# Kernel optimization log

Hardware: AMD Instinct MI355X
Metric: run time of the kernel (lower is better)

## Reference

```python
import jax, jax.numpy as jnp
import numpy as np

E = 512
H = 8
D = E // H  # 64
B = 2
S = 4096


def setup_inputs() -> dict:
    key = jax.random.key(0)
    ks = jax.random.split(key, 12)
    s = 1.0 / np.sqrt(E)
    return {
        "x": jax.random.normal(ks[0], (B, S, E), dtype=jnp.float32),
        "bias": jax.random.normal(ks[1], (H, 1, S, S), dtype=jnp.float32),
        "mask": jax.random.randint(ks[2], (1, 1, S, S), 0, 2, dtype=jnp.int32),
        "Wq": jax.random.normal(ks[3], (E, E), dtype=jnp.float32) * s,
        "bq": jnp.zeros((E,), dtype=jnp.float32),
        "Wk": jax.random.normal(ks[4], (E, E), dtype=jnp.float32) * s,
        "bk": jnp.zeros((E,), dtype=jnp.float32),
        "Wv": jax.random.normal(ks[5], (E, E), dtype=jnp.float32) * s,
        "bv": jnp.zeros((E,), dtype=jnp.float32),
        "Wo": jax.random.normal(ks[6], (E, E), dtype=jnp.float32) * s,
        "bo": jnp.zeros((E,), dtype=jnp.float32),
    }


def _split_heads(t):
    # [B,S,E] -> [H,B,S,D]  (matches x.view(B,-1,H,D).permute(2,0,1,3))
    b, s, _ = t.shape
    return t.reshape(b, s, H, D).transpose(2, 0, 1, 3)


def reference(x, bias, mask, Wq, bq, Wk, bk, Wv, bv, Wo, bo):
    # torch Linear: y = x @ W.T + b
    q = _split_heads(x @ Wq.T + bq)  # [H,B,S,D]
    k = _split_heads(x @ Wk.T + bk)
    v = _split_heads(x @ Wv.T + bv)

    scores = jnp.einsum("hbqd,hbkd->hbqk", q, k) + bias  # [H,B,S,S]
    scores = jnp.where(mask == 0, jnp.float32(-1e20), scores)
    # NOTE: original divides AFTER bias-add and masking
    probs = jax.nn.softmax(scores / jnp.sqrt(jnp.float32(D)), axis=-1)
    out = jnp.einsum("hbqk,hbkd->hbqd", probs, v)  # [H,B,S,D]
    out = out.transpose(1, 2, 0, 3).reshape(x.shape[0], -1, H * D)  # [B,S,E]
    return out @ Wo.T + bo
```

## Files before the change

kernel.cpp:

```cpp
#include <hip/hip_runtime.h>
#include <hip/hip_bf16.h>

typedef __bf16 bf16x8 __attribute__((ext_vector_type(8)));
typedef float f32x4 __attribute__((ext_vector_type(4)));

#define S_LEN 4096
#define EMB   512
#define NHEAD 8
#define HDIM  64
#define NBAT  2
#define NROW  (NBAT * S_LEN)

static __device__ __forceinline__ f32x4 mfma16x16(bf16x8 a, bf16x8 b, f32x4 c) {
    return __builtin_amdgcn_mfma_f32_16x16x32_bf16(a, b, c, 0, 0, 0);
}

__global__ __launch_bounds__(256) void convert_kernel(
    const float* __restrict__ x, const float* __restrict__ Wq,
    const float* __restrict__ Wk, const float* __restrict__ Wv,
    const float* __restrict__ Wo,
    __hip_bfloat16* __restrict__ xb, __hip_bfloat16* __restrict__ wqkv,
    __hip_bfloat16* __restrict__ wob)
{
    const int NX = NROW * EMB;
    const int NW = EMB * EMB;
    int i = blockIdx.x * 256 + threadIdx.x;
    if (i < NX) { xb[i] = __float2bfloat16(x[i]); return; }
    int j = i - NX;
    if (j < 3 * NW) {
        int p = j >> 18, r = j & (NW - 1);
        const float* src = (p == 0) ? Wq : (p == 1) ? Wk : Wv;
        wqkv[j] = __float2bfloat16(src[r]);
    } else if (j < 4 * NW) {
        int r = j - 3 * NW;
        wob[r] = __float2bfloat16(Wo[r]);
    }
}

__device__ __forceinline__ void gemm_core(
    const __hip_bfloat16* __restrict__ A, const __hip_bfloat16* __restrict__ Bw,
    int mbase, int nbase,
    __hip_bfloat16* As, __hip_bfloat16* Bs, f32x4 acc[2][4])
{
    const int tid = threadIdx.x;
    const int w = tid >> 6, lane = tid & 63, l = lane & 15, quad = lane >> 4;
    const f32x4 zero = {0.f, 0.f, 0.f, 0.f};
#pragma unroll
    for (int mb = 0; mb < 2; mb++)
#pragma unroll
        for (int nb = 0; nb < 4; nb++) acc[mb][nb] = zero;

    const int r0 = tid >> 2, kc = tid & 3;
    const __hip_bfloat16* pa0 = A + (size_t)(mbase + r0) * EMB + kc * 8;
    const __hip_bfloat16* pa1 = pa0 + (size_t)64 * EMB;
    const __hip_bfloat16* pb  = Bw + (size_t)(nbase + r0) * EMB + kc * 8;

    uint4 va0 = *(const uint4*)pa0;
    uint4 va1 = *(const uint4*)pa1;
    uint4 vb  = *(const uint4*)pb;

    for (int k0 = 0; k0 < EMB; k0 += 32) {
        __syncthreads();
        *(uint4*)(As + r0 * 40 + kc * 8)        = va0;
        *(uint4*)(As + (r0 + 64) * 40 + kc * 8) = va1;
        *(uint4*)(Bs + r0 * 40 + kc * 8)        = vb;
        __syncthreads();
        if (k0 + 32 < EMB) {
            va0 = *(const uint4*)(pa0 + k0 + 32);
            va1 = *(const uint4*)(pa1 + k0 + 32);
            vb  = *(const uint4*)(pb  + k0 + 32);
        }
        bf16x8 af[2], bfr[4];
#pragma unroll
        for (int mb = 0; mb < 2; mb++)
            af[mb] = *(const bf16x8*)(As + (w * 32 + mb * 16 + l) * 40 + quad * 8);
#pragma unroll
        for (int nb = 0; nb < 4; nb++)
            bfr[nb] = *(const bf16x8*)(Bs + (nb * 16 + l) * 40 + quad * 8);
        __builtin_amdgcn_s_setprio(1);
#pragma unroll
        for (int mb = 0; mb < 2; mb++)
#pragma unroll
            for (int nb = 0; nb < 4; nb++)
                acc[mb][nb] = mfma16x16(af[mb], bfr[nb], acc[mb][nb]);
        __builtin_amdgcn_s_setprio(0);
    }
}

__global__ __launch_bounds__(256, 4) void qkv_gemm(
    const __hip_bfloat16* __restrict__ xb, const __hip_bfloat16* __restrict__ wqkv,
    const float* __restrict__ bq, const float* __restrict__ bk, const float* __restrict__ bv,
    __hip_bfloat16* __restrict__ Qh, __hip_bfloat16* __restrict__ Kh,
    __hip_bfloat16* __restrict__ Vt)
{
    __shared__ __align__(16) __hip_bfloat16 As[128 * 40];
    __shared__ __align__(16) __hip_bfloat16 Bs[64 * 40];
    const int mbase = blockIdx.x * 128, nbase = blockIdx.y * 64;
    f32x4 acc[2][4];
    gemm_core(xb, wqkv, mbase, nbase, As, Bs, acc);

    const int tid = threadIdx.x;
    const int w = tid >> 6, lane = tid & 63, l = lane & 15, quad = lane >> 4;
    const int p = nbase >> 9;
    const float* bias = (p == 0) ? bq : (p == 1) ? bk : bv;
    __hip_bfloat16* dst = (p == 0) ? Qh : (p == 1) ? Kh : Vt;
#pragma unroll
    for (int mb = 0; mb < 2; mb++)
#pragma unroll
        for (int nb = 0; nb < 4; nb++)
#pragma unroll
            for (int r = 0; r < 4; r++) {
                int m = mbase + w * 32 + mb * 16 + quad * 4 + r;
                int n = nbase + nb * 16 + l;
                int o = n & 511;
                float v = acc[mb][nb][r] + bias[o];
                int b = m >> 12, s = m & 4095, hh = o >> 6, d = o & 63;
                size_t idx = (p == 2)
                    ? ((size_t)((hh * 2 + b) * 64 + d)) * 4096 + s
                    : ((size_t)((hh * 2 + b) * 4096 + s)) * 64 + d;
                dst[idx] = __float2bfloat16(v);
            }
}

__global__ __launch_bounds__(256, 2) void attn_kernel(
    const __hip_bfloat16* __restrict__ Qh, const __hip_bfloat16* __restrict__ Kh,
    const __hip_bfloat16* __restrict__ Vt,
    const float* __restrict__ bias, const int* __restrict__ mask,
    __hip_bfloat16* __restrict__ Om)
{
    const int h = blockIdx.x, qt = blockIdx.y;
    const int tid = threadIdx.x;
    const int w = tid >> 6, lane = tid & 63, l = lane & 15, quad = lane >> 4;
    const int q0 = qt * 64;
    const float CS = 0.18033688011112042f;

    __shared__ __align__(16) __hip_bfloat16 Ks[2][64 * 72];
    __shared__ __align__(16) __hip_bfloat16 Vs[2][64 * 72];
    __shared__ __align__(16) __hip_bfloat16 Ps[64 * 72];

    bf16x8 qf[2][2];
#pragma unroll
    for (int b = 0; b < 2; b++) {
        const __hip_bfloat16* qp =
            Qh + ((size_t)((h * 2 + b) * 4096 + q0 + w * 16 + l)) * 64;
        qf[b][0] = *(const bf16x8*)(qp + quad * 8);
        qf[b][1] = *(const bf16x8*)(qp + 32 + quad * 8);
    }

    f32x4 oacc[2][4];
    float mst[2][4], lst[2][4];
    const f32x4 zero = {0.f, 0.f, 0.f, 0.f};
#pragma unroll
    for (int b = 0; b < 2; b++) {
#pragma unroll
        for (int nb = 0; nb < 4; nb++) oacc[b][nb] = zero;
#pragma unroll
        for (int r = 0; r < 4; r++) { mst[b][r] = -__builtin_inff(); lst[b][r] = 0.f; }
    }

    const __hip_bfloat16* kvsrc[8];
    __hip_bfloat16* kvdst[8];
#pragma unroll
    for (int j = 0; j < 8; j++) {
        int c = j * 256 + tid;
        int t = c >> 9, b = t & 1, isV = t >> 1;
        int cc = c & 511, row = cc >> 3, ch = cc & 7;
        if (isV) {
            kvsrc[j] = Vt + ((size_t)((h * 2 + b) * 64 + row)) * 4096 + ch * 8;
            kvdst[j] = Vs[b] + row * 72 + ch * 8;
        } else {
            kvsrc[j] = Kh + ((size_t)((h * 2 + b) * 4096 + row)) * 64 + ch * 8;
            kvdst[j] = Ks[b] + row * 72 + ch * 8;
        }
    }
    const float* bptr[4];
    const int*   mptr[4];
#pragma unroll
    for (int r = 0; r < 4; r++) {
        int qq = q0 + w * 16 + quad * 4 + r;
        bptr[r] = bias + (size_t)h * S_LEN * S_LEN + (size_t)qq * S_LEN + l;
        mptr[r] = mask + (size_t)qq * S_LEN + l;
    }

    uint4 kvbuf[8];
    float bb[4][4];
    int   mm[4][4];
#pragma unroll
    for (int j = 0; j < 8; j++) {
        kvbuf[j] = *(const uint4*)kvsrc[j];
        kvsrc[j] += (j >> 2) ? 64 : 64 * 64;
    }
#pragma unroll
    for (int nb = 0; nb < 4; nb++)
#pragma unroll
        for (int r = 0; r < 4; r++) {
            bb[nb][r] = bptr[r][nb * 16];
            mm[nb][r] = mptr[r][nb * 16];
        }
#pragma unroll
    for (int r = 0; r < 4; r++) { bptr[r] += 64; mptr[r] += 64; }

    for (int kt = 0; kt < 64; kt++) {
        __syncthreads();
#pragma unroll
        for (int j = 0; j < 8; j++) *(uint4*)kvdst[j] = kvbuf[j];
        float bor[4][4];
#pragma unroll
        for (int nb = 0; nb < 4; nb++)
#pragma unroll
            for (int r = 0; r < 4; r++)
                bor[nb][r] = mm[nb][r] ? bb[nb][r] : -1e30f;
        __syncthreads();

        if (kt < 63) {
#pragma unroll
            for (int j = 0; j < 8; j++) {
                kvbuf[j] = *(const uint4*)kvsrc[j];
                kvsrc[j] += (j >> 2) ? 64 : 64 * 64;
            }
#pragma unroll
            for (int nb = 0; nb < 4; nb++)
#pragma unroll
                for (int r = 0; r < 4; r++) {
                    bb[nb][r] = bptr[r][nb * 16];
                    mm[nb][r] = mptr[r][nb * 16];
                }
#pragma unroll
            for (int r = 0; r < 4; r++) { bptr[r] += 64; mptr[r] += 64; }
        }

#pragma unroll
        for (int b = 0; b < 2; b++) {
            f32x4 sc[4] = {zero, zero, zero, zero};
            __builtin_amdgcn_s_setprio(1);
#pragma unroll
            for (int ks = 0; ks < 2; ks++)
#pragma unroll
                for (int nb = 0; nb < 4; nb++) {
                    bf16x8 kf = *(const bf16x8*)(Ks[b] + (nb * 16 + l) * 72 + ks * 32 + quad * 8);
                    sc[nb] = mfma16x16(qf[b][ks], kf, sc[nb]);
                }
            __builtin_amdgcn_s_setprio(0);
            float xv[4][4], rmax[4];
#pragma unroll
            for (int r = 0; r < 4; r++) rmax[r] = -__builtin_inff();
#pragma unroll
            for (int nb = 0; nb < 4; nb++)
#pragma unroll
                for (int r = 0; r < 4; r++) {
                    xv[nb][r] = (sc[nb][r] + bor[nb][r]) * CS;
                    rmax[r] = fmaxf(rmax[r], xv[nb][r]);
                }
#pragma unroll
            for (int r = 0; r < 4; r++) {
                rmax[r] = fmaxf(rmax[r], __shfl_xor(rmax[r], 1));
                rmax[r] = fmaxf(rmax[r], __shfl_xor(rmax[r], 2));
                rmax[r] = fmaxf(rmax[r], __shfl_xor(rmax[r], 4));
                rmax[r] = fmaxf(rmax[r], __shfl_xor(rmax[r], 8));
            }
            float alpha[4], rsum[4];
#pragma unroll
            for (int r = 0; r < 4; r++) {
                float mn = fmaxf(mst[b][r], rmax[r]);
                alpha[r] = __builtin_amdgcn_exp2f(mst[b][r] - mn);
                mst[b][r] = mn;
                rsum[r] = 0.f;
            }
#pragma unroll
            for (int nb = 0; nb < 4; nb++)
#pragma unroll
                for (int r = 0; r < 4; r++) {
                    float e = __builtin_amdgcn_exp2f(xv[nb][r] - mst[b][r]);
                    rsum[r] += e;
                    Ps[(w * 16 + quad * 4 + r) * 72 + nb * 16 + l] =
                        __float2bfloat16(e);
                }
#pragma unroll
            for (int r = 0; r < 4; r++) {
                rsum[r] += __shfl_xor(rsum[r], 1);
                rsum[r] += __shfl_xor(rsum[r], 2);
                rsum[r] += __shfl_xor(rsum[r], 4);
                rsum[r] += __shfl_xor(rsum[r], 8);
                lst[b][r] = lst[b][r] * alpha[r] + rsum[r];
            }
#pragma unroll
            for (int nb = 0; nb < 4; nb++)
#pragma unroll
                for (int r = 0; r < 4; r++) oacc[b][nb][r] *= alpha[r];
            __builtin_amdgcn_s_setprio(1);
#pragma unroll
            for (int ks = 0; ks < 2; ks++) {
                bf16x8 pf = *(const bf16x8*)(Ps + (w * 16 + l) * 72 + ks * 32 + quad * 8);
#pragma unroll
                for (int nb = 0; nb < 4; nb++) {
                    bf16x8 vf = *(const bf16x8*)(Vs[b] + (nb * 16 + l) * 72 + ks * 32 + quad * 8);
                    oacc[b][nb] = mfma16x16(pf, vf, oacc[b][nb]);
                }
            }
            __builtin_amdgcn_s_setprio(0);
        }
    }

#pragma unroll
    for (int b = 0; b < 2; b++)
#pragma unroll
        for (int nb = 0; nb < 4; nb++)
#pragma unroll
            for (int r = 0; r < 4; r++) {
                int qq = q0 + w * 16 + quad * 4 + r;
                float val = oacc[b][nb][r] / lst[b][r];
                Om[((size_t)(b * 4096 + qq)) * 512 + h * 64 + nb * 16 + l] =
                    __float2bfloat16(val);
            }
}

__global__ __launch_bounds__(256, 4) void out_gemm(
    const __hip_bfloat16* __restrict__ Om, const __hip_bfloat16* __restrict__ wob,
    const float* __restrict__ bo, float* __restrict__ out)
{
    __shared__ __align__(16) __hip_bfloat16 As[128 * 40];
    __shared__ __align__(16) __hip_bfloat16 Bs[64 * 40];
    const int mbase = blockIdx.x * 128, nbase = blockIdx.y * 64;
    f32x4 acc[2][4];
    gemm_core(Om, wob, mbase, nbase, As, Bs, acc);

    const int tid = threadIdx.x;
    const int w = tid >> 6, lane = tid & 63, l = lane & 15, quad = lane >> 4;
#pragma unroll
    for (int mb = 0; mb < 2; mb++)
#pragma unroll
        for (int nb = 0; nb < 4; nb++)
#pragma unroll
            for (int r = 0; r < 4; r++) {
                int m = mbase + w * 32 + mb * 16 + quad * 4 + r;
                int n = nbase + nb * 16 + l;
                out[(size_t)m * EMB + n] = acc[mb][nb][r] + bo[n];
            }
}

extern "C" void kernel_launch(void* const* d_in, const int* in_sizes, int n_in,
                              void* d_out, int out_size, void* d_ws, size_t ws_size,
                              hipStream_t stream) {
    const float* x    = (const float*)d_in[0];
    const float* bias = (const float*)d_in[1];
    const int*   mask = (const int*)d_in[2];
    const float* Wq   = (const float*)d_in[3];
    const float* bq   = (const float*)d_in[4];
    const float* Wk   = (const float*)d_in[5];
    const float* bk   = (const float*)d_in[6];
    const float* Wv   = (const float*)d_in[7];
    const float* bv   = (const float*)d_in[8];
    const float* Wo   = (const float*)d_in[9];
    const float* bo   = (const float*)d_in[10];
    float* out = (float*)d_out;

    char* ws = (char*)d_ws;
    __hip_bfloat16* xb   = (__hip_bfloat16*)ws; ws += (size_t)NROW * EMB * 2;
    __hip_bfloat16* wqkv = (__hip_bfloat16*)ws; ws += (size_t)3 * EMB * EMB * 2;
    __hip_bfloat16* wob  = (__hip_bfloat16*)ws; ws += (size_t)EMB * EMB * 2;
    __hip_bfloat16* Qh   = (__hip_bfloat16*)ws; ws += (size_t)NROW * EMB * 2;
    __hip_bfloat16* Kh   = (__hip_bfloat16*)ws; ws += (size_t)NROW * EMB * 2;
    __hip_bfloat16* Vt   = (__hip_bfloat16*)ws; ws += (size_t)NROW * EMB * 2;
    __hip_bfloat16* Om   = (__hip_bfloat16*)ws; ws += (size_t)NROW * EMB * 2;

    convert_kernel<<<dim3(20480), dim3(256), 0, stream>>>(
        x, Wq, Wk, Wv, Wo, xb, wqkv, wob);
    qkv_gemm<<<dim3(64, 24), dim3(256), 0, stream>>>(
        xb, wqkv, bq, bk, bv, Qh, Kh, Vt);
    attn_kernel<<<dim3(NHEAD, 64), dim3(256), 0, stream>>>(
        Qh, Kh, Vt, bias, mask, Om);
    out_gemm<<<dim3(64, 8), dim3(256), 0, stream>>>(Om, wob, bo, out);
}
```

Measured before the change: 1.261 ms.

## Stage bias and mask through LDS with vectorized float4 loads

```diff
diff --git a/kernel.cpp b/kernel.cpp
--- a/kernel.cpp
+++ b/kernel.cpp
@@ -137,6 +137,7 @@
     __shared__ __align__(16) __hip_bfloat16 Ks[2][64 * 72];
     __shared__ __align__(16) __hip_bfloat16 Vs[2][64 * 72];
     __shared__ __align__(16) __hip_bfloat16 Ps[64 * 72];
+    __shared__ __align__(16) float Bor[64 * 68];
 
     bf16x8 qf[2][2];
 #pragma unroll
@@ -158,76 +159,78 @@
         for (int r = 0; r < 4; r++) { mst[b][r] = -__builtin_inff(); lst[b][r] = 0.f; }
     }
 
-    const __hip_bfloat16* kvsrc[8];
-    __hip_bfloat16* kvdst[8];
+    const int krow = tid >> 3, kch = tid & 7;
+    const int ldso0 = krow * 72 + kch * 8;
+    const int ldso1 = ldso0 + 32 * 72;
+    int koff[8];
 #pragma unroll
     for (int j = 0; j < 8; j++) {
-        int c = j * 256 + tid;
-        int t = c >> 9, b = t & 1, isV = t >> 1;
-        int cc = c & 511, row = cc >> 3, ch = cc & 7;
-        if (isV) {
-            kvsrc[j] = Vt + ((size_t)((h * 2 + b) * 64 + row)) * 4096 + ch * 8;
-            kvdst[j] = Vs[b] + row * 72 + ch * 8;
-        } else {
-            kvsrc[j] = Kh + ((size_t)((h * 2 + b) * 4096 + row)) * 64 + ch * 8;
-            kvdst[j] = Ks[b] + row * 72 + ch * 8;
-        }
-    }
-    const float* bptr[4];
-    const int*   mptr[4];
-#pragma unroll
-    for (int r = 0; r < 4; r++) {
-        int qq = q0 + w * 16 + quad * 4 + r;
-        bptr[r] = bias + (size_t)h * S_LEN * S_LEN + (size_t)qq * S_LEN + l;
-        mptr[r] = mask + (size_t)qq * S_LEN + l;
-    }
-
-    uint4 kvbuf[8];
-    float bb[4][4];
-    int   mm[4][4];
-#pragma unroll
-    for (int j = 0; j < 8; j++) {
-        kvbuf[j] = *(const uint4*)kvsrc[j];
-        kvsrc[j] += (j >> 2) ? 64 : 64 * 64;
-    }
-#pragma unroll
-    for (int nb = 0; nb < 4; nb++)
-#pragma unroll
-        for (int r = 0; r < 4; r++) {
-            bb[nb][r] = bptr[r][nb * 16];
-            mm[nb][r] = mptr[r][nb * 16];
-        }
-#pragma unroll
-    for (int r = 0; r < 4; r++) { bptr[r] += 64; mptr[r] += 64; }
+        int b = (j >> 1) & 1, isV = j >> 2;
+        int row = (j & 1) * 32 + krow;
+        koff[j] = isV
+            ? ((h * 2 + b) * 64 + row) * 4096 + kch * 8
+            : ((h * 2 + b) * 4096 + row) * 64 + kch * 8;
+    }
+    const float* biasH = bias + (size_t)h * S_LEN * S_LEN;
+    int bmo[4], bro[4];
+#pragma unroll
+    for (int j = 0; j < 4; j++) {
+        int d = j * 256 + tid, row = d >> 4, c4 = d & 15;
+        bmo[j] = (q0 + row) * S_LEN + c4 * 4;
+        bro[j] = row * 68 + c4 * 4;
+    }
+
+    uint4  kv[8];
+    float4 bv4[4];
+    int4   mv4[4];
+#pragma unroll
+    for (int j = 0; j < 8; j++)
+        kv[j] = (j >> 2) ? *(const uint4*)(Vt + koff[j])
+                         : *(const uint4*)(Kh + koff[j]);
+#pragma unroll
+    for (int j = 0; j < 4; j++) {
+        bv4[j] = *(const float4*)(biasH + bmo[j]);
+        mv4[j] = *(const int4*)(mask + bmo[j]);
+    }
 
     for (int kt = 0; kt < 64; kt++) {
         __syncthreads();
 #pragma unroll
-        for (int j = 0; j < 8; j++) *(uint4*)kvdst[j] = kvbuf[j];
-        float bor[4][4];
+        for (int j = 0; j < 8; j++) {
+            int lo = (j & 1) ? ldso1 : ldso0;
+            if (j >> 2) *(uint4*)(Vs[(j >> 1) & 1] + lo) = kv[j];
+            else        *(uint4*)(Ks[(j >> 1) & 1] + lo) = kv[j];
+        }
+#pragma unroll
+        for (int j = 0; j < 4; j++) {
+            float4 t;
+            t.x = mv4[j].x ? bv4[j].x * CS : -1e30f;
+            t.y = mv4[j].y ? bv4[j].y * CS : -1e30f;
+            t.z = mv4[j].z ? bv4[j].z * CS : -1e30f;
+            t.w = mv4[j].w ? bv4[j].w * CS : -1e30f;
+            *(float4*)(Bor + bro[j]) = t;
+        }
+        __syncthreads();
+
+        if (kt < 63) {
+            const int k0 = (kt + 1) * 64;
+#pragma unroll
+            for (int j = 0; j < 8; j++)
+                kv[j] = (j >> 2) ? *(const uint4*)(Vt + koff[j] + k0)
+                                 : *(const uint4*)(Kh + koff[j] + k0 * 64);
+#pragma unroll
+            for (int j = 0; j < 4; j++) {
+                bv4[j] = *(const float4*)(biasH + bmo[j] + k0);
+                mv4[j] = *(const int4*)(mask + bmo[j] + k0);
+            }
+        }
+
+        float borr[4][4];
 #pragma unroll
         for (int nb = 0; nb < 4; nb++)
 #pragma unroll
             for (int r = 0; r < 4; r++)
-                bor[nb][r] = mm[nb][r] ? bb[nb][r] : -1e30f;
-        __syncthreads();
-
-        if (kt < 63) {
-#pragma unroll
-            for (int j = 0; j < 8; j++) {
-                kvbuf[j] = *(const uint4*)kvsrc[j];
-                kvsrc[j] += (j >> 2) ? 64 : 64 * 64;
-            }
-#pragma unroll
-            for (int nb = 0; nb < 4; nb++)
-#pragma unroll
-                for (int r = 0; r < 4; r++) {
-                    bb[nb][r] = bptr[r][nb * 16];
-                    mm[nb][r] = mptr[r][nb * 16];
-                }
-#pragma unroll
-            for (int r = 0; r < 4; r++) { bptr[r] += 64; mptr[r] += 64; }
-        }
+                borr[nb][r] = Bor[(w * 16 + quad * 4 + r) * 68 + nb * 16 + l];
 
 #pragma unroll
         for (int b = 0; b < 2; b++) {
@@ -248,7 +251,7 @@
             for (int nb = 0; nb < 4; nb++)
 #pragma unroll
                 for (int r = 0; r < 4; r++) {
-                    xv[nb][r] = (sc[nb][r] + bor[nb][r]) * CS;
+                    xv[nb][r] = fmaf(sc[nb][r], CS, borr[nb][r]);
                     rmax[r] = fmaxf(rmax[r], xv[nb][r]);
                 }
 #pragma unroll
```

After: 1.179 ms. -6.6%, faster.
